# Performance work log

Hardware: AMD Instinct MI355X
Metric: run time of the kernel (lower is better)

## Reference

```python
import jax, jax.numpy as jnp
import numpy as np

B, N, C = 4, 8192, 256
E = 262144
OUT = 256  # out_ch * heads = 128 * 2


def setup_inputs() -> dict:
    key = jax.random.key(0)
    ks = jax.random.split(key, 6)
    x = jax.random.normal(ks[0], (B, N, C), dtype=jnp.float32)
    edge_index = jax.random.randint(ks[1], (2, E), 0, N, dtype=jnp.int64)
    s = 1.0 / np.sqrt(C)
    W_self = jax.random.normal(ks[2], (C, OUT), dtype=jnp.float32) * s
    b_self = jax.random.normal(ks[3], (OUT,), dtype=jnp.float32) * 0.01
    W_neigh = jax.random.normal(ks[4], (C, OUT), dtype=jnp.float32) * s
    b_neigh = jax.random.normal(ks[5], (OUT,), dtype=jnp.float32) * 0.01
    return {"x": x, "edge_index": edge_index, "W_self": W_self, "b_self": b_self,
            "W_neigh": W_neigh, "b_neigh": b_neigh}


def _build_A_hat(edge_index, n):
    # A[i,j] = multiplicity of edge (src=i, dst=j), plus self loops (identity),
    # matching torch.sparse_coo_tensor(...).to_dense() which sums duplicates.
    src, dst = edge_index[0], edge_index[1]
    A = jnp.zeros((n, n), dtype=jnp.float32).at[src, dst].add(1.0)
    A = A + jnp.eye(n, dtype=jnp.float32)
    deg = jnp.clip(A.sum(axis=1), 1.0, None)  # [N]
    return A / deg[:, None]  # row-normalized adjacency


def reference(x, edge_index, W_self, b_self, W_neigh, b_neigh):
    n = x.shape[1]
    A_hat = _build_A_hat(edge_index, n)            # [N, N]
    h_self = x @ W_self + b_self                   # [B, N, OUT]
    y = jnp.einsum('ij,bjc->bic', A_hat, x)        # neighbor aggregation
    h_nei = y @ W_neigh + b_neigh                  # [B, N, OUT]
    return jax.nn.gelu(h_self + h_nei, approximate=False)
```

## Files before the change

### kernel.cpp

```cpp
#include <hip/hip_runtime.h>
#include <math.h>

#define BB 4
#define NN 8192
#define CC 256
#define OUTC 256
#define EE 262144
#define MROWS (BB*NN)
#define CAP 96

typedef __attribute__((ext_vector_type(8))) short short8;
typedef __attribute__((ext_vector_type(4))) short s16x4;
typedef __attribute__((ext_vector_type(4))) float f32x4;
typedef __attribute__((ext_vector_type(2))) unsigned int u32x2;
typedef __attribute__((ext_vector_type(4))) unsigned int u32x4;

__device__ inline unsigned short f2bf(float f) {
    union { float f; unsigned u; } a; a.f = f;
    unsigned u = a.u;
    u += 0x7fffu + ((u >> 16) & 1u);
    return (unsigned short)(u >> 16);
}
__device__ inline float bf2f(unsigned short h) {
    union { unsigned u; float f; } a; a.u = ((unsigned)h) << 16;
    return a.f;
}
__device__ inline float asf(unsigned u) {
    union { unsigned u; float f; } a; a.u = u;
    return a.f;
}
__device__ inline float gelu1(float v) {
    float t = v * (0.7978845608f + 0.0356774081f * v * v);
    float e = __expf(2.0f * t);
    float th = 1.0f - 2.0f / (e + 1.0f);
    return 0.5f * v * (1.0f + th);
}


__global__ __launch_bounds__(256) void prep_w(const float* __restrict__ Ws,
                                              const float* __restrict__ Wn,
                                              unsigned short* __restrict__ Wt2,
                                              int* __restrict__ cnt) {
    int bi = blockIdx.x;
    int tid = threadIdx.x;
    if (bi >= 32) {
        cnt[(bi - 32) * 256 + tid] = 0;
        return;
    }
    __shared__ float tile[64][65];
    int kt = bi >> 3, nt = bi & 7;
    int k0 = kt * 64, n0 = nt * 64;
    const float* W = (n0 < 256) ? Ws : Wn;
    int ncol = n0 & 255;
#pragma unroll
    for (int p = 0; p < 4; p++) {
        int krow = p * 16 + (tid >> 4);
        int col = (tid & 15) * 4;
        float4 v = *(const float4*)&W[(size_t)(k0 + krow) * 256 + ncol + col];
        tile[krow][col + 0] = v.x;
        tile[krow][col + 1] = v.y;
        tile[krow][col + 2] = v.z;
        tile[krow][col + 3] = v.w;
    }
    __syncthreads();
#pragma unroll
    for (int e = 0; e < 2; e++) {
        int idx = e * 256 + tid;
        int lane = idx & 63;
        int ni = (idx >> 6) & 3;
        int kkl = idx >> 8;
        int kk = kt * 2 + kkl;
        int qrow = lane >> 4, fr = lane & 15;
        short8 t;
#pragma unroll
        for (int j = 0; j < 8; j++)
            t[j] = (short)f2bf(tile[kkl * 32 + qrow * 8 + j][ni * 16 + fr]);
        *(short8*)&Wt2[(size_t)(((nt * 8 + kk) * 4 + ni) * 512) + lane * 8] = t;
    }
}


#define APAD 8
#define ALD (256 + APAD)

__global__ __launch_bounds__(256, 2) void gemm_fill(const float* __restrict__ X,
                                                    const unsigned short* __restrict__ Wt2,
                                                    unsigned short* __restrict__ Zb,
                                                    unsigned short* __restrict__ U,
                                                    const int* __restrict__ ei,
                                                    int* __restrict__ cnt,
                                                    unsigned short* __restrict__ adjb) {
    __shared__ unsigned short sA[64 * ALD];
    int bi = blockIdx.x;
    int tid = threadIdx.x;

    if (bi < 256) {
        int e = bi * 256 + tid;
        for (; e < EE; e += 256 * 256) {
            int s = ei[e] & (NN - 1);
            int d = ei[EE + e] & (NN - 1);
            int slot = atomicAdd(&cnt[s], 1);
            if (slot < CAP) adjb[(size_t)s * CAP + slot] = (unsigned short)d;
        }
        return;
    }

    int wave = tid >> 6, lane = tid & 63;
    int row0 = (bi - 256) * 64;
    int qrow = lane >> 4;
    int fr = lane & 15;

#pragma unroll
    for (int q = 0; q < 16; q++) {
        int f = q * 1024 + tid * 4;
        int rr = f >> 8, k0 = f & 255;
        float4 v = *(const float4*)&X[(size_t)(row0 + rr) * 256 + k0];
        s16x4 t;
        t[0] = (short)f2bf(v.x); t[1] = (short)f2bf(v.y);
        t[2] = (short)f2bf(v.z); t[3] = (short)f2bf(v.w);
        *(s16x4*)&sA[rr * ALD + k0] = t;
    }
    __syncthreads();

#pragma unroll 1
    for (int sp = 0; sp < 2; sp++) {
        int colbase = wave * 128 + sp * 64;
        int ct = wave * 2 + sp;
        const unsigned short* Bp = Wt2 + (size_t)ct * 8 * 4 * 512 + lane * 8;

        f32x4 acc[4][4];
#pragma unroll
        for (int ni = 0; ni < 4; ni++)
#pragma unroll
            for (int mi = 0; mi < 4; mi++) acc[ni][mi] = (f32x4)0.0f;

        short8 bbuf[3][4];
#pragma unroll
        for (int ni = 0; ni < 4; ni++) {
            bbuf[0][ni] = *(const short8*)&Bp[(size_t)(0 * 4 + ni) * 512];
            bbuf[1][ni] = *(const short8*)&Bp[(size_t)(1 * 4 + ni) * 512];
        }

#pragma unroll
        for (int kk = 0; kk < 8; kk++) {
            if (kk < 6) {
#pragma unroll
                for (int ni = 0; ni < 4; ni++)
                    bbuf[(kk + 2) % 3][ni] =
                        *(const short8*)&Bp[(size_t)((kk + 2) * 4 + ni) * 512];
            }
            int ak = kk * 32 + qrow * 8;
            short8 af[4];
#pragma unroll
            for (int mi = 0; mi < 4; mi++)
                af[mi] = *(const short8*)&sA[(mi * 16 + fr) * ALD + ak];
#pragma unroll
            for (int ni = 0; ni < 4; ni++)
#pragma unroll
                for (int mi = 0; mi < 4; mi++)
                    acc[ni][mi] = __builtin_amdgcn_mfma_f32_16x16x32_bf16(
                        bbuf[kk % 3][ni], af[mi], acc[ni][mi], 0, 0, 0);
        }

#pragma unroll
        for (int mi = 0; mi < 4; mi++) {
            size_t row = (size_t)(row0 + mi * 16 + fr);
#pragma unroll
            for (int ni = 0; ni < 4; ni++) {
                int col = colbase + ni * 16 + qrow * 4;
                s16x4 t;
                t[0] = (short)f2bf(acc[ni][mi][0]);
                t[1] = (short)f2bf(acc[ni][mi][1]);
                t[2] = (short)f2bf(acc[ni][mi][2]);
                t[3] = (short)f2bf(acc[ni][mi][3]);
                if (colbase < 256) *(s16x4*)&Zb[row * 512 + 256 + col] = t;
                else               *(s16x4*)&U[row * 256 + (col - 256)] = t;
            }
        }
    }
}


__global__ __launch_bounds__(256) void agg_gelu(const unsigned short* __restrict__ U,
                                                const int* __restrict__ cnt,
                                                const unsigned short* __restrict__ adjb,
                                                const float* __restrict__ bs,
                                                const float* __restrict__ bn,
                                                float* __restrict__ Out) {
    int r = blockIdx.x & 7;
    int q = blockIdx.x >> 3;
    int b = r & 3;
    int g = ((r >> 2) << 10) + q;
    int i = (g << 2) + (threadIdx.x >> 6);
    i = __builtin_amdgcn_readfirstlane(i);
    int lane = threadIdx.x & 63;
    int l5 = lane & 31;
    int sub = lane >> 5;
    int cb = l5 * 8;
    int c_out = cb + sub * 4;

    const unsigned short* Ub = U + (size_t)b * NN * 256;
    size_t row = (size_t)b * NN + i;

    int deg = cnt[i];
    int m = min(deg, CAP);
    int P = m & 1;
    int K = (m + 1) >> 1;
    const unsigned* lp = (const unsigned*)(adjb + (size_t)i * CAP);

    const unsigned* ZbP = (const unsigned*)Out;
    u32x2 zz = __builtin_nontemporal_load((const u32x2*)&ZbP[row * 256 + 128 + (c_out >> 1)]);
    float4 vs = *(const float4*)&bs[c_out];
    float4 vn = *(const float4*)&bn[c_out];
    u32x4 sv4 = *(const u32x4*)(Ub + (size_t)i * 256 + cb);

    float a[8];
    unsigned smask = (sub == 0 && P == 0) ? 0xffffffffu : 0u;
#pragma unroll
    for (int d = 0; d < 4; d++) {
        unsigned x = sv4[d] & smask;
        a[2 * d]     = asf(x << 16);
        a[2 * d + 1] = asf(x & 0xffff0000u);
    }

    int p = 0;
    for (; p + 8 <= K; p += 8) {
        unsigned w[8];
#pragma unroll
        for (int t = 0; t < 8; t++) w[t] = lp[p + t];
        u32x4 v4[8];
#pragma unroll
        for (int t = 0; t < 8; t++) {
            unsigned lo = w[t] & 0xffffu;
            unsigned hi = w[t] >> 16;
            hi = (2 * (p + t) + 1 < m) ? hi : (unsigned)i;
            unsigned j = sub ? hi : lo;
            v4[t] = *(const u32x4*)(Ub + (size_t)j * 256 + cb);
        }
#pragma unroll
        for (int t = 0; t < 8; t++) {
#pragma unroll
            for (int d = 0; d < 4; d++) {
                a[2 * d]     += asf(v4[t][d] << 16);
                a[2 * d + 1] += asf(v4[t][d] & 0xffff0000u);
            }
        }
    }
    for (; p < K; p++) {
        unsigned w = lp[p];
        unsigned lo = w & 0xffffu;
        unsigned hi = w >> 16;
        hi = (2 * p + 1 < m) ? hi : (unsigned)i;
        unsigned j = sub ? hi : lo;
        u32x4 v4 = *(const u32x4*)(Ub + (size_t)j * 256 + cb);
#pragma unroll
        for (int d = 0; d < 4; d++) {
            a[2 * d]     += asf(v4[d] << 16);
            a[2 * d + 1] += asf(v4[d] & 0xffff0000u);
        }
    }

#pragma unroll
    for (int k = 0; k < 8; k++) a[k] += __shfl_xor(a[k], 32);

    float r0 = sub ? a[4] : a[0];
    float r1 = sub ? a[5] : a[1];
    float r2 = sub ? a[6] : a[2];
    float r3 = sub ? a[7] : a[3];

    float z0 = bf2f((unsigned short)(zz[0] & 0xffff));
    float z1 = bf2f((unsigned short)(zz[0] >> 16));
    float z2 = bf2f((unsigned short)(zz[1] & 0xffff));
    float z3 = bf2f((unsigned short)(zz[1] >> 16));

    float s = 1.0f / (float)(1 + deg);
    float v0 = z0 + vs.x + vn.x + s * r0;
    float v1 = z1 + vs.y + vn.y + s * r1;
    float v2 = z2 + vs.z + vn.z + s * r2;
    float v3 = z3 + vs.w + vn.w + s * r3;

    f32x4 gout;
    gout[0] = gelu1(v0);
    gout[1] = gelu1(v1);
    gout[2] = gelu1(v2);
    gout[3] = gelu1(v3);
    __builtin_nontemporal_store(gout, (f32x4*)&Out[row * 256 + c_out]);
}


extern "C" void kernel_launch(void* const* d_in, const int* in_sizes, int n_in,
                              void* d_out, int out_size, void* d_ws, size_t ws_size,
                              hipStream_t stream) {
    const float* x   = (const float*)d_in[0];
    const int* ei    = (const int*)d_in[1];
    const float* Ws  = (const float*)d_in[2];
    const float* bsv = (const float*)d_in[3];
    const float* Wn  = (const float*)d_in[4];
    const float* bnv = (const float*)d_in[5];
    float* out = (float*)d_out;

    char* ws = (char*)d_ws;
    size_t o = 0;
    unsigned short* U   = (unsigned short*)(ws + o); o += (size_t)MROWS * OUTC * 2;
    unsigned short* Wt2 = (unsigned short*)(ws + o); o += (size_t)512 * 256 * 2;
    int* cnt = (int*)(ws + o);  o += (size_t)NN * 4;
    unsigned short* adjb = (unsigned short*)(ws + o); o += (size_t)NN * CAP * 2;

    prep_w<<<64, 256, 0, stream>>>(Ws, Wn, Wt2, cnt);

    gemm_fill<<<768, 256, 0, stream>>>(x, Wt2, (unsigned short*)out, U, ei, cnt, adjb);

    agg_gelu<<<8192, 256, 0, stream>>>(U, cnt, adjb, bsv, bnv, out);
}
```

Before: 143.5 us.

## Split aggregation across channel halves with four neighbor groups per wave

The aggregation kernel now launches twice as many blocks, and each handles half the output channels. Within a wave, four 16-lane groups each gather a different neighbor row, and the partial sums are reduced with two xor shuffles. The self-projection bf16 buffer moves out of the output tensor into its own workspace array, so each block can read it without colliding with the output writes. This aims to raise memory-level parallelism and occupancy for the gather, at the cost of extra shuffles, redundant lanes that do not store, and an extra 16 MB workspace buffer.

```diff
diff --git a/kernel.cpp b/kernel.cpp
--- a/kernel.cpp
+++ b/kernel.cpp
@@ -173,7 +173,7 @@
                 t[1] = (short)f2bf(acc[ni][mi][1]);
                 t[2] = (short)f2bf(acc[ni][mi][2]);
                 t[3] = (short)f2bf(acc[ni][mi][3]);
-                if (colbase < 256) *(s16x4*)&Zb[row * 512 + 256 + col] = t;
+                if (colbase < 256) *(s16x4*)&Zb[row * 256 + col] = t;
                 else               *(s16x4*)&U[row * 256 + (col - 256)] = t;
             }
         }
@@ -186,36 +186,38 @@
                                                 const unsigned short* __restrict__ adjb,
                                                 const float* __restrict__ bs,
                                                 const float* __restrict__ bn,
-                                                float* __restrict__ Out) {
-    int r = blockIdx.x & 7;
-    int q = blockIdx.x >> 3;
+                                                float* __restrict__ Out,
+                                                const unsigned short* __restrict__ Zb) {
+    int blk = blockIdx.x;
+    int half = blk >> 13;
+    int blk13 = blk & 8191;
+    int r = blk13 & 7;
     int b = r & 3;
-    int g = ((r >> 2) << 10) + q;
-    int i = (g << 2) + (threadIdx.x >> 6);
+    int g2 = ((r >> 2) << 10) + (blk13 >> 3);
+    int i = (g2 << 2) + (threadIdx.x >> 6);
     i = __builtin_amdgcn_readfirstlane(i);
     int lane = threadIdx.x & 63;
-    int l5 = lane & 31;
-    int sub = lane >> 5;
-    int cb = l5 * 8;
-    int c_out = cb + sub * 4;
+    int grp = lane >> 4;
+    int li = lane & 15;
+    int cb = half * 128 + li * 8;
+    int ge = grp & 1;
+    int c_out = cb + ge * 4;
 
     const unsigned short* Ub = U + (size_t)b * NN * 256;
     size_t row = (size_t)b * NN + i;
 
     int deg = cnt[i];
     int m = min(deg, CAP);
-    int P = m & 1;
-    int K = (m + 1) >> 1;
     const unsigned* lp = (const unsigned*)(adjb + (size_t)i * CAP);
 
-    const unsigned* ZbP = (const unsigned*)Out;
-    u32x2 zz = __builtin_nontemporal_load((const u32x2*)&ZbP[row * 256 + 128 + (c_out >> 1)]);
+    const u32x2* Zq = (const u32x2*)(Zb + row * 256);
+    u32x2 zz = __builtin_nontemporal_load(&Zq[c_out >> 2]);
     float4 vs = *(const float4*)&bs[c_out];
     float4 vn = *(const float4*)&bn[c_out];
     u32x4 sv4 = *(const u32x4*)(Ub + (size_t)i * 256 + cb);
 
     float a[8];
-    unsigned smask = (sub == 0 && P == 0) ? 0xffffffffu : 0u;
+    unsigned smask = (grp == 0) ? 0xffffffffu : 0u;
 #pragma unroll
     for (int d = 0; d < 4; d++) {
         unsigned x = sv4[d] & smask;
@@ -224,21 +226,19 @@
     }
 
     int p = 0;
-    for (; p + 8 <= K; p += 8) {
+    for (; p + 16 <= m; p += 16) {
         unsigned w[8];
 #pragma unroll
-        for (int t = 0; t < 8; t++) w[t] = lp[p + t];
-        u32x4 v4[8];
-#pragma unroll
-        for (int t = 0; t < 8; t++) {
-            unsigned lo = w[t] & 0xffffu;
-            unsigned hi = w[t] >> 16;
-            hi = (2 * (p + t) + 1 < m) ? hi : (unsigned)i;
-            unsigned j = sub ? hi : lo;
+        for (int t = 0; t < 8; t++) w[t] = lp[(p >> 1) + t];
+        u32x4 v4[4];
+#pragma unroll
+        for (int t = 0; t < 4; t++) {
+            unsigned dw = w[2 * t + (grp >> 1)];
+            unsigned j = ge ? (dw >> 16) : (dw & 0xffffu);
             v4[t] = *(const u32x4*)(Ub + (size_t)j * 256 + cb);
         }
 #pragma unroll
-        for (int t = 0; t < 8; t++) {
+        for (int t = 0; t < 4; t++) {
 #pragma unroll
             for (int d = 0; d < 4; d++) {
                 a[2 * d]     += asf(v4[t][d] << 16);
@@ -246,27 +246,33 @@
             }
         }
     }
-    for (; p < K; p++) {
-        unsigned w = lp[p];
-        unsigned lo = w & 0xffffu;
-        unsigned hi = w >> 16;
-        hi = (2 * p + 1 < m) ? hi : (unsigned)i;
-        unsigned j = sub ? hi : lo;
+    for (; p < m; p += 4) {
+        unsigned w0 = lp[p >> 1];
+        unsigned w1 = lp[(p >> 1) + 1];
+        int slot = p + grp;
+        unsigned dw = (grp >> 1) ? w1 : w0;
+        unsigned j = ge ? (dw >> 16) : (dw & 0xffffu);
+        unsigned msk = (slot < m) ? 0xffffffffu : 0u;
+        j = (slot < m) ? j : (unsigned)i;
         u32x4 v4 = *(const u32x4*)(Ub + (size_t)j * 256 + cb);
 #pragma unroll
         for (int d = 0; d < 4; d++) {
-            a[2 * d]     += asf(v4[d] << 16);
-            a[2 * d + 1] += asf(v4[d] & 0xffff0000u);
-        }
-    }
-
-#pragma unroll
-    for (int k = 0; k < 8; k++) a[k] += __shfl_xor(a[k], 32);
-
-    float r0 = sub ? a[4] : a[0];
-    float r1 = sub ? a[5] : a[1];
-    float r2 = sub ? a[6] : a[2];
-    float r3 = sub ? a[7] : a[3];
+            unsigned x = v4[d] & msk;
+            a[2 * d]     += asf(x << 16);
+            a[2 * d + 1] += asf(x & 0xffff0000u);
+        }
+    }
+
+#pragma unroll
+    for (int k = 0; k < 8; k++) {
+        a[k] += __shfl_xor(a[k], 16);
+        a[k] += __shfl_xor(a[k], 32);
+    }
+
+    float r0 = ge ? a[4] : a[0];
+    float r1 = ge ? a[5] : a[1];
+    float r2 = ge ? a[6] : a[2];
+    float r3 = ge ? a[7] : a[3];
 
     float z0 = bf2f((unsigned short)(zz[0] & 0xffff));
     float z1 = bf2f((unsigned short)(zz[0] >> 16));
@@ -274,17 +280,13 @@
     float z3 = bf2f((unsigned short)(zz[1] >> 16));
 
     float s = 1.0f / (float)(1 + deg);
-    float v0 = z0 + vs.x + vn.x + s * r0;
-    float v1 = z1 + vs.y + vn.y + s * r1;
-    float v2 = z2 + vs.z + vn.z + s * r2;
-    float v3 = z3 + vs.w + vn.w + s * r3;
-
     f32x4 gout;
-    gout[0] = gelu1(v0);
-    gout[1] = gelu1(v1);
-    gout[2] = gelu1(v2);
-    gout[3] = gelu1(v3);
-    __builtin_nontemporal_store(gout, (f32x4*)&Out[row * 256 + c_out]);
+    gout[0] = gelu1(z0 + vs.x + vn.x + s * r0);
+    gout[1] = gelu1(z1 + vs.y + vn.y + s * r1);
+    gout[2] = gelu1(z2 + vs.z + vn.z + s * r2);
+    gout[3] = gelu1(z3 + vs.w + vn.w + s * r3);
+    if (grp < 2)
+        __builtin_nontemporal_store(gout, (f32x4*)&Out[row * 256 + c_out]);
 }
 
 
@@ -302,13 +304,14 @@
     char* ws = (char*)d_ws;
     size_t o = 0;
     unsigned short* U   = (unsigned short*)(ws + o); o += (size_t)MROWS * OUTC * 2;
+    unsigned short* Zb  = (unsigned short*)(ws + o); o += (size_t)MROWS * OUTC * 2;
     unsigned short* Wt2 = (unsigned short*)(ws + o); o += (size_t)512 * 256 * 2;
     int* cnt = (int*)(ws + o);  o += (size_t)NN * 4;
     unsigned short* adjb = (unsigned short*)(ws + o); o += (size_t)NN * CAP * 2;
 
     prep_w<<<64, 256, 0, stream>>>(Ws, Wn, Wt2, cnt);
 
-    gemm_fill<<<768, 256, 0, stream>>>(x, Wt2, (unsigned short*)out, U, ei, cnt, adjb);
-
-    agg_gelu<<<8192, 256, 0, stream>>>(U, cnt, adjb, bsv, bnv, out);
-}
+    gemm_fill<<<768, 256, 0, stream>>>(x, Wt2, Zb, U, ei, cnt, adjb);
+
+    agg_gelu<<<16384, 256, 0, stream>>>(U, cnt, adjb, bsv, bnv, out, Zb);
+}
```

Result: slower. 156.0 us (+8.7%).
